# Optimization experiments

Hardware: AMD Instinct MI355X
Metric: run time of the kernel (lower is better)

The kernel has to match this reference:

```python
import jax, jax.numpy as jnp
import numpy as np

N, K, F_DIM, D = 50000, 20, 256, 128


def setup_inputs() -> dict:
    key = jax.random.key(0)
    ks = jax.random.split(key, 8)
    s = 0.05  # small init scale for numerical stability
    return {
        "h": jax.random.normal(ks[0], (N, F_DIM), dtype=jnp.float32),
        "aggregate_neighbors": jax.random.randint(ks[1], (N, K), 0, N),
        "W_past": jax.random.normal(ks[2], (F_DIM, D), dtype=jnp.float32) * s,
        "W": jax.random.normal(ks[3], (2 * D, D), dtype=jnp.float32) * s,
        "W_ih": jax.random.normal(ks[4], (4 * D, D), dtype=jnp.float32) * s,
        "W_hh": jax.random.normal(ks[5], (4 * D, D), dtype=jnp.float32) * s,
        "b_ih": jax.random.normal(ks[6], (4 * D,), dtype=jnp.float32) * s,
        "b_hh": jax.random.normal(ks[7], (4 * D,), dtype=jnp.float32) * s,
    }


def _lstm(seq, W_ih, W_hh, b_ih, b_hh):
    # seq: (N, K, D) batch_first single-layer LSTM; returns final (h_n, c_n), each (N, D)
    n, _, d = seq.shape

    def step(carry, x_t):
        h_t, c_t = carry
        gates = x_t @ W_ih.T + b_ih + h_t @ W_hh.T + b_hh  # (N, 4D)
        i, f, g, o = jnp.split(gates, 4, axis=-1)
        c = jax.nn.sigmoid(f) * c_t + jax.nn.sigmoid(i) * jnp.tanh(g)
        h_new = jax.nn.sigmoid(o) * jnp.tanh(c)
        return (h_new, c), None

    init = (jnp.zeros((n, d), seq.dtype), jnp.zeros((n, d), seq.dtype))
    (h_n, c_n), _ = jax.lax.scan(step, init, jnp.swapaxes(seq, 0, 1))
    return h_n, c_n


def reference(h, aggregate_neighbors, W_past, W, W_ih, W_hh, b_ih, b_hh):
    hp = h @ W_past                      # (N, D) projected features
    seq = hp[aggregate_neighbors]        # (N, K, D) per-node neighbor gather
    h_n, c_n = _lstm(seq, W_ih, W_hh, b_ih, b_hh)
    neigh = jnp.concatenate([hp, h_n], axis=1)  # (N, 2D)
    out = jax.nn.elu(neigh @ W)          # (N, D)
    return out, h_n, c_n
```

## Files before the change

### kernel.cpp

```cpp
#include <hip/hip_runtime.h>

#define NN 50000
#define KSEQ 20
#define HN_OFF 6400000
#define CN_OFF 12800000

using short8 = __attribute__((ext_vector_type(8))) short;
using f32x4  = __attribute__((ext_vector_type(4))) float;

__device__ __forceinline__ unsigned short f2bf(float f) {
    unsigned int u = __float_as_uint(f);
    return (unsigned short)((u + 0x7FFFu + ((u >> 16) & 1u)) >> 16);
}
__device__ __forceinline__ float exp2x(float x) { float r; asm("v_exp_f32 %0, %1" : "=v"(r) : "v"(x)); return r; }
__device__ __forceinline__ float rcpx(float x)  { float r; asm("v_rcp_f32 %0, %1" : "=v"(r) : "v"(x)); return r; }

#define L2E 1.4426950408889634f
__device__ __forceinline__ float sigp(float y)  { return rcpx(1.f + exp2x(y)); }
__device__ __forceinline__ float tanhp(float y) { return fmaf(-2.f, rcpx(1.f + exp2x(y)), 1.f); }

__global__ void prep_kernel(const float* __restrict__ Wp, const float* __restrict__ W,
                            const float* __restrict__ Wih, const float* __restrict__ Whh,
                            const float* __restrict__ bih, const float* __restrict__ bhh,
                            unsigned short* __restrict__ Wih_b, unsigned short* __restrict__ Whh_b,
                            unsigned short* __restrict__ Wpt, unsigned short* __restrict__ Wtt,
                            float* __restrict__ bsum) {
    int tid = blockIdx.x * blockDim.x + threadIdx.x;
    if (tid < 65536) {
        float sc = ((tid >> 14) == 2) ? (2.f * L2E) : (-L2E);
        Wih_b[tid] = f2bf(Wih[tid] * sc); return;
    }
    tid -= 65536;
    if (tid < 65536) {
        float sc = ((tid >> 14) == 2) ? (2.f * L2E) : (-L2E);
        Whh_b[tid] = f2bf(Whh[tid] * sc); return;
    }
    tid -= 65536;
    if (tid < 32768) { int j = tid >> 8, k = tid & 255; Wpt[tid] = f2bf(Wp[k * 128 + j]); return; }
    tid -= 32768;
    if (tid < 32768) { int j = tid >> 8, k = tid & 255; Wtt[tid] = f2bf(W[k * 128 + j]); return; }
    tid -= 32768;
    if (tid < 512) {
        float sc = ((tid >> 7) == 2) ? (2.f * L2E) : (-L2E);
        bsum[tid] = (bih[tid] + bhh[tid]) * sc;
    }
}

__global__ __launch_bounds__(512, 2) void hp_g_kernel(const float* __restrict__ h,
                                                      const unsigned short* __restrict__ Wpt,
                                                      const unsigned short* __restrict__ Wih_b,
                                                      const float* __restrict__ bsum,
                                                      unsigned short* __restrict__ hp_bf,
                                                      unsigned short* __restrict__ G) {
    __shared__ __align__(16) unsigned char smem[24576];
    const int tid = threadIdx.x;
    const int w = tid >> 6, l = tid & 63;
    const int l15 = l & 15, lq = l >> 4;
    const int base = blockIdx.x * 32;
    const int colj = w * 16 + l15;

#pragma unroll
    for (int i = 0; i < 4; ++i) {
        int chunk = tid + 512 * i;
        int row = chunk >> 6, kc = chunk & 63;
        int grow = base + row;
        float4 v = make_float4(0.f, 0.f, 0.f, 0.f);
        if (grow < NN) v = *(const float4*)(h + (size_t)grow * 256 + kc * 4);
        ushort4 bv = make_ushort4(f2bf(v.x), f2bf(v.y), f2bf(v.z), f2bf(v.w));
        int off = (row * 512 + kc * 8) ^ ((row & 7) << 4);
        *(ushort4*)(smem + off) = bv;
    }
    __syncthreads();

    short8 bf[8];
#pragma unroll
    for (int kt = 0; kt < 8; ++kt)
        bf[kt] = *(const short8*)((const unsigned char*)Wpt + colj * 512 + kt * 64 + lq * 16);

    f32x4 acc[2];
    acc[0] = (f32x4){0.f, 0.f, 0.f, 0.f};
    acc[1] = acc[0];
#pragma unroll
    for (int kt = 0; kt < 8; ++kt) {
#pragma unroll
        for (int rt = 0; rt < 2; ++rt) {
            int arow = rt * 16 + l15;
            int off = (arow * 512 + kt * 64 + lq * 16) ^ ((arow & 7) << 4);
            short8 a = *(const short8*)(smem + off);
            acc[rt] = __builtin_amdgcn_mfma_f32_16x16x32_bf16(a, bf[kt], acc[rt], 0, 0, 0);
        }
    }
#pragma unroll
    for (int rt = 0; rt < 2; ++rt)
#pragma unroll
        for (int r = 0; r < 4; ++r) {
            int row = rt * 16 + lq * 4 + r;
            int grow = base + row;
            unsigned short hb = f2bf(acc[rt][r]);
            if (grow < NN) hp_bf[(size_t)grow * 128 + colj] = hb;
            *(unsigned short*)(smem + 16384 + ((row * 256 + colj * 2) ^ ((row & 7) << 4))) = hb;
        }
    __syncthreads();

    short8 bw4[4][4];
    float bi[4];
#pragma unroll
    for (int g = 0; g < 4; ++g) {
#pragma unroll
        for (int kt = 0; kt < 4; ++kt)
            bw4[g][kt] = *(const short8*)((const unsigned char*)Wih_b + (g * 128 + colj) * 256 + kt * 64 + lq * 16);
        bi[g] = bsum[g * 128 + colj];
    }
    const int off0 = (l15 * 256 + lq * 16) ^ ((l15 & 7) << 4);

    f32x4 ag[4][2];
#pragma unroll
    for (int g = 0; g < 4; ++g) { ag[g][0] = (f32x4){bi[g], bi[g], bi[g], bi[g]}; ag[g][1] = ag[g][0]; }
#pragma unroll
    for (int kt = 0; kt < 4; ++kt)
#pragma unroll
        for (int rt = 0; rt < 2; ++rt) {
            short8 a = *(const short8*)(smem + 16384 + rt * 4096 + (off0 ^ (kt << 6)));
#pragma unroll
            for (int g = 0; g < 4; ++g)
                ag[g][rt] = __builtin_amdgcn_mfma_f32_16x16x32_bf16(a, bw4[g][kt], ag[g][rt], 0, 0, 0);
        }
#pragma unroll
    for (int rt = 0; rt < 2; ++rt)
#pragma unroll
        for (int e = 0; e < 4; ++e) {
            int grow = base + rt * 16 + lq * 4 + e;
            if (grow < NN) {
                ushort4 pk = make_ushort4(f2bf(ag[0][rt][e]), f2bf(ag[1][rt][e]),
                                          f2bf(ag[2][rt][e]), f2bf(ag[3][rt][e]));
                *(ushort4*)(G + (size_t)grow * 512 + colj * 4) = pk;
            }
        }
}

#define SLAB 12288
template<int RP>
__device__ __forceinline__ void lstm_step(unsigned char* lds, int t,
    uint2 (&gx)[4], const short8 (&bw)[4][4], f32x4& cst,
    const unsigned char* Gp, const unsigned cb,
    const int off0, const int colj, const int lq, const int hwb, const int hswz,
    const int base, float* __restrict__ out)
{
    constexpr int NP = RP ^ 1;
    int4 idx4;
    if (t < KSEQ - 1)
        idx4 = *(const int4*)(lds + SLAB + (t + 1) * 64 + lq * 16);

    f32x4 acc[4];
#pragma unroll
    for (int e = 0; e < 4; ++e) {
        uint2 u = gx[e];
        acc[0][e] = __uint_as_float(u.x << 16);
        acc[1][e] = __uint_as_float(u.x & 0xFFFF0000u);
        acc[2][e] = __uint_as_float(u.y << 16);
        acc[3][e] = __uint_as_float(u.y & 0xFFFF0000u);
    }
    if (t < KSEQ - 1) {
        gx[0] = *(const uint2*)(Gp + (((unsigned)idx4.x << 10) + cb));
        gx[1] = *(const uint2*)(Gp + (((unsigned)idx4.y << 10) + cb));
        gx[2] = *(const uint2*)(Gp + (((unsigned)idx4.z << 10) + cb));
        gx[3] = *(const uint2*)(Gp + (((unsigned)idx4.w << 10) + cb));
    }
    if (t > 0) {
        __builtin_amdgcn_s_setprio(1);
#pragma unroll
        for (int kt = 0; kt < 4; ++kt) {
            short8 a = *(const short8*)(lds + RP * 4096 + (off0 ^ (kt << 6)));
#pragma unroll
            for (int g = 0; g < 4; ++g)
                acc[g] = __builtin_amdgcn_mfma_f32_16x16x32_bf16(a, bw[g][kt], acc[g], 0, 0, 0);
        }
        __builtin_amdgcn_s_setprio(0);
    }
#pragma unroll
    for (int e = 0; e < 4; ++e) {
        float Ai = 1.f + exp2x(acc[0][e]);
        float Af = 1.f + exp2x(acc[1][e]);
        float B  = 1.f + exp2x(acc[2][e]);
        float AiB = Ai * B;
        float c = fmaf(cst[e], AiB, Af * (B - 2.f)) * rcpx(Af * AiB);
        cst[e] = c;
        float C  = 1.f + exp2x((2.f * L2E) * c);
        float Do = 1.f + exp2x(acc[3][e]);
        float hv = (C - 2.f) * rcpx(C * Do);
        unsigned pk;
        asm("v_cvt_pk_bf16_f32 %0, %1, %2" : "=v"(pk) : "v"(hv), "v"(hv));
        *(unsigned short*)(lds + NP * 4096 + ((hwb + e * 256) ^ (hswz ^ (e << 4)))) = (unsigned short)pk;
        if (t == KSEQ - 1) {
            int grow = base + lq * 4 + e;
            out[HN_OFF + (size_t)grow * 128 + colj] = hv;
            out[CN_OFF + (size_t)grow * 128 + colj] = c;
        }
    }
    __syncthreads();
}

__global__ __launch_bounds__(512, 4) void lstm_kernel(const unsigned short* __restrict__ hp_bf,
                                                      const int* __restrict__ agg,
                                                      const unsigned short* __restrict__ G,
                                                      const unsigned short* __restrict__ Whh_b,
                                                      const unsigned short* __restrict__ Wtt,
                                                      float* __restrict__ out) {
    __shared__ __align__(16) unsigned char lds[14336];
    const int tid = threadIdx.x;
    const int w = tid >> 6, l = tid & 63;
    const int l15 = l & 15, lq = l >> 4;
    const int base = blockIdx.x * 16;
    const int colj = w * 16 + l15;

    if (tid < 256) {
        int row = tid >> 4, c = tid & 15;
        uint4 v = *(const uint4*)((const unsigned char*)hp_bf + (size_t)(base + row) * 256 + c * 16);
        *(uint4*)(lds + 8192 + ((row * 256 + c * 16) ^ ((row & 7) << 4))) = v;
    }
    if (tid < 320) {
        int row = tid / 20, t = tid - row * 20;
        *(int*)(lds + SLAB + t * 64 + row * 4) = agg[(size_t)base * KSEQ + tid];
    }

    short8 bw[4][4];
#pragma unroll
    for (int g = 0; g < 4; ++g)
#pragma unroll
        for (int kt = 0; kt < 4; ++kt)
            bw[g][kt] = *(const short8*)((const unsigned char*)Whh_b + (g * 128 + colj) * 256 + kt * 64 + lq * 16);

    const int off0 = (l15 * 256 + lq * 16) ^ ((l15 & 7) << 4);
    const int hwb = lq * 1024 + colj * 2;
    const int hswz = (lq & 1) << 6;
    const unsigned char* Gp = (const unsigned char*)G;
    const unsigned cb = (unsigned)colj * 8;

    f32x4 cst = (f32x4){0.f, 0.f, 0.f, 0.f};
    __syncthreads();

    uint2 gx[4];
    {
        int4 i4 = *(const int4*)(lds + SLAB + lq * 16);
        gx[0] = *(const uint2*)(Gp + (((unsigned)i4.x << 10) + cb));
        gx[1] = *(const uint2*)(Gp + (((unsigned)i4.y << 10) + cb));
        gx[2] = *(const uint2*)(Gp + (((unsigned)i4.z << 10) + cb));
        gx[3] = *(const uint2*)(Gp + (((unsigned)i4.w << 10) + cb));
    }

#pragma unroll 1
    for (int tt = 0; tt < KSEQ; tt += 2) {
        lstm_step<0>(lds, tt,     gx, bw, cst, Gp, cb, off0, colj, lq, hwb, hswz, base, out);
        lstm_step<1>(lds, tt + 1, gx, bw, cst, Gp, cb, off0, colj, lq, hwb, hswz, base, out);
    }

    short8 bo[8];
#pragma unroll
    for (int kt = 0; kt < 8; ++kt)
        bo[kt] = *(const short8*)((const unsigned char*)Wtt + colj * 512 + kt * 64 + lq * 16);

    f32x4 a2 = (f32x4){0.f, 0.f, 0.f, 0.f};
#pragma unroll
    for (int kt = 0; kt < 4; ++kt) {
        short8 a = *(const short8*)(lds + 8192 + (off0 ^ (kt << 6)));
        a2 = __builtin_amdgcn_mfma_f32_16x16x32_bf16(a, bo[kt], a2, 0, 0, 0);
    }
#pragma unroll
    for (int kt = 0; kt < 4; ++kt) {
        short8 a = *(const short8*)(lds + (off0 ^ (kt << 6)));
        a2 = __builtin_amdgcn_mfma_f32_16x16x32_bf16(a, bo[kt + 4], a2, 0, 0, 0);
    }
#pragma unroll
    for (int e = 0; e < 4; ++e) {
        int grow = base + lq * 4 + e;
        float v = a2[e];
        out[(size_t)grow * 128 + colj] = (v > 0.f) ? v : (exp2x(L2E * v) - 1.f);
    }
}

extern "C" void kernel_launch(void* const* d_in, const int* in_sizes, int n_in,
                              void* d_out, int out_size, void* d_ws, size_t ws_size,
                              hipStream_t stream) {
    (void)in_sizes; (void)n_in; (void)out_size; (void)ws_size;
    const float* h   = (const float*)d_in[0];
    const int*   agg = (const int*)d_in[1];
    const float* Wp  = (const float*)d_in[2];
    const float* W   = (const float*)d_in[3];
    const float* Wih = (const float*)d_in[4];
    const float* Whh = (const float*)d_in[5];
    const float* bih = (const float*)d_in[6];
    const float* bhh = (const float*)d_in[7];
    float* out = (float*)d_out;

    unsigned short* hp_bf = (unsigned short*)d_ws;
    unsigned short* G     = hp_bf + 6400000;
    unsigned short* Wih_b = G + 25600000;
    unsigned short* Whh_b = Wih_b + 65536;
    unsigned short* Wpt   = Whh_b + 65536;
    unsigned short* Wtt   = Wpt + 32768;
    float*          bsum  = (float*)(Wtt + 32768);

    prep_kernel<<<771, 256, 0, stream>>>(Wp, W, Wih, Whh, bih, bhh, Wih_b, Whh_b, Wpt, Wtt, bsum);
    hp_g_kernel<<<1563, 512, 0, stream>>>(h, Wpt, Wih_b, bsum, hp_bf, G);
    lstm_kernel<<<3125, 512, 0, stream>>>(hp_bf, agg, G, Whh_b, Wtt, out);
}
```

Measured before the change: 283.4 us.

## Prefetch gathered input-gate rows into LDS via async global_load_lds

The per-step gather of precomputed input-gate rows G now goes through global_load_lds into double-buffered LDS slabs. Each wave fetches whole 1KB rows for two neighbor indices, and the step reads its slice back from LDS. Before, each thread issued four scattered 8-byte register loads. The goal is to replace many small scattered loads with coalesced 16-byte-per-lane row loads that run asynchronously, overlapping the next step's gather with the current step's compute. It also makes the output stores nontemporal. LDS use rises from about 14KB to about 49KB per block, which may cut occupancy below the 4-blocks-per-CU launch bound.

```diff
diff --git a/kernel.cpp b/kernel.cpp
--- a/kernel.cpp
+++ b/kernel.cpp
@@ -18,6 +18,12 @@
 #define L2E 1.4426950408889634f
 __device__ __forceinline__ float sigp(float y)  { return rcpx(1.f + exp2x(y)); }
 __device__ __forceinline__ float tanhp(float y) { return fmaf(-2.f, rcpx(1.f + exp2x(y)), 1.f); }
+
+typedef const __attribute__((address_space(1))) unsigned int gu32;
+typedef __attribute__((address_space(3))) unsigned int lu32;
+__device__ __forceinline__ void gload_lds16(const void* g, void* l) {
+    __builtin_amdgcn_global_load_lds((gu32*)g, (lu32*)l, 16, 0, 0);
+}
 
 __global__ void prep_kernel(const float* __restrict__ Wp, const float* __restrict__ W,
                             const float* __restrict__ Wih, const float* __restrict__ Whh,
@@ -139,32 +145,32 @@
 }
 
 #define SLAB 12288
+#define GXB  16384
+#define GXP  1040
+#define GXS  16640
+
 template<int RP>
 __device__ __forceinline__ void lstm_step(unsigned char* lds, int t,
-    uint2 (&gx)[4], const short8 (&bw)[4][4], f32x4& cst,
-    const unsigned char* Gp, const unsigned cb,
+    const short8 (&bw)[4][4], f32x4& cst,
+    const unsigned char* Gpl, const int slabw, const int gxw, const int gxr,
     const int off0, const int colj, const int lq, const int hwb, const int hswz,
     const int base, float* __restrict__ out)
 {
     constexpr int NP = RP ^ 1;
-    int4 idx4;
-    if (t < KSEQ - 1)
-        idx4 = *(const int4*)(lds + SLAB + (t + 1) * 64 + lq * 16);
-
+    if (t < KSEQ - 1) {
+        int i0 = *(const int*)(lds + slabw + (t + 1) * 64);
+        int i1 = *(const int*)(lds + slabw + (t + 1) * 64 + 4);
+        gload_lds16(Gpl + ((size_t)(unsigned)i0 << 10), lds + gxw + NP * GXS);
+        gload_lds16(Gpl + ((size_t)(unsigned)i1 << 10), lds + gxw + NP * GXS + GXP);
+    }
     f32x4 acc[4];
 #pragma unroll
     for (int e = 0; e < 4; ++e) {
-        uint2 u = gx[e];
+        uint2 u = *(const uint2*)(lds + gxr + RP * GXS + e * GXP);
         acc[0][e] = __uint_as_float(u.x << 16);
         acc[1][e] = __uint_as_float(u.x & 0xFFFF0000u);
         acc[2][e] = __uint_as_float(u.y << 16);
         acc[3][e] = __uint_as_float(u.y & 0xFFFF0000u);
-    }
-    if (t < KSEQ - 1) {
-        gx[0] = *(const uint2*)(Gp + (((unsigned)idx4.x << 10) + cb));
-        gx[1] = *(const uint2*)(Gp + (((unsigned)idx4.y << 10) + cb));
-        gx[2] = *(const uint2*)(Gp + (((unsigned)idx4.z << 10) + cb));
-        gx[3] = *(const uint2*)(Gp + (((unsigned)idx4.w << 10) + cb));
     }
     if (t > 0) {
         __builtin_amdgcn_s_setprio(1);
@@ -193,8 +199,8 @@
         *(unsigned short*)(lds + NP * 4096 + ((hwb + e * 256) ^ (hswz ^ (e << 4)))) = (unsigned short)pk;
         if (t == KSEQ - 1) {
             int grow = base + lq * 4 + e;
-            out[HN_OFF + (size_t)grow * 128 + colj] = hv;
-            out[CN_OFF + (size_t)grow * 128 + colj] = c;
+            __builtin_nontemporal_store(hv, &out[HN_OFF + (size_t)grow * 128 + colj]);
+            __builtin_nontemporal_store(c,  &out[CN_OFF + (size_t)grow * 128 + colj]);
         }
     }
     __syncthreads();
@@ -206,7 +212,7 @@
                                                       const unsigned short* __restrict__ Whh_b,
                                                       const unsigned short* __restrict__ Wtt,
                                                       float* __restrict__ out) {
-    __shared__ __align__(16) unsigned char lds[14336];
+    __shared__ __align__(16) unsigned char lds[GXB + 2 * GXS];
     const int tid = threadIdx.x;
     const int w = tid >> 6, l = tid & 63;
     const int l15 = l & 15, lq = l >> 4;
@@ -222,6 +228,18 @@
         int row = tid / 20, t = tid - row * 20;
         *(int*)(lds + SLAB + t * 64 + row * 4) = agg[(size_t)base * KSEQ + tid];
     }
+    __syncthreads();
+
+    const unsigned char* Gpl = (const unsigned char*)G + l * 16;
+    const int slabw = SLAB + w * 8;
+    const int gxw   = GXB + w * 2080;
+
+    {
+        int i0 = *(const int*)(lds + slabw);
+        int i1 = *(const int*)(lds + slabw + 4);
+        gload_lds16(Gpl + ((size_t)(unsigned)i0 << 10), lds + gxw);
+        gload_lds16(Gpl + ((size_t)(unsigned)i1 << 10), lds + gxw + GXP);
+    }
 
     short8 bw[4][4];
 #pragma unroll
@@ -233,25 +251,15 @@
     const int off0 = (l15 * 256 + lq * 16) ^ ((l15 & 7) << 4);
     const int hwb = lq * 1024 + colj * 2;
     const int hswz = (lq & 1) << 6;
-    const unsigned char* Gp = (const unsigned char*)G;
-    const unsigned cb = (unsigned)colj * 8;
+    const int gxr = GXB + lq * (4 * GXP) + colj * 8;
 
     f32x4 cst = (f32x4){0.f, 0.f, 0.f, 0.f};
     __syncthreads();
-
-    uint2 gx[4];
-    {
-        int4 i4 = *(const int4*)(lds + SLAB + lq * 16);
-        gx[0] = *(const uint2*)(Gp + (((unsigned)i4.x << 10) + cb));
-        gx[1] = *(const uint2*)(Gp + (((unsigned)i4.y << 10) + cb));
-        gx[2] = *(const uint2*)(Gp + (((unsigned)i4.z << 10) + cb));
-        gx[3] = *(const uint2*)(Gp + (((unsigned)i4.w << 10) + cb));
-    }
 
 #pragma unroll 1
     for (int tt = 0; tt < KSEQ; tt += 2) {
-        lstm_step<0>(lds, tt,     gx, bw, cst, Gp, cb, off0, colj, lq, hwb, hswz, base, out);
-        lstm_step<1>(lds, tt + 1, gx, bw, cst, Gp, cb, off0, colj, lq, hwb, hswz, base, out);
+        lstm_step<0>(lds, tt,     bw, cst, Gpl, slabw, gxw, gxr, off0, colj, lq, hwb, hswz, base, out);
+        lstm_step<1>(lds, tt + 1, bw, cst, Gpl, slabw, gxw, gxr, off0, colj, lq, hwb, hswz, base, out);
     }
 
     short8 bo[8];
@@ -274,7 +282,8 @@
     for (int e = 0; e < 4; ++e) {
         int grow = base + lq * 4 + e;
         float v = a2[e];
-        out[(size_t)grow * 128 + colj] = (v > 0.f) ? v : (exp2x(L2E * v) - 1.f);
+        v = (v > 0.f) ? v : (exp2x(L2E * v) - 1.f);
+        __builtin_nontemporal_store(v, &out[(size_t)grow * 128 + colj]);
     }
 }
 
```

Measured after the change: 282.0 us (median of 2 runs). Within noise of the previous version (-0.5%).
